# Performance work log

Hardware: AMD Instinct MI355X
Metric: run time of the kernel (lower is better)

The kernel has to match this reference:

```python
import jax, jax.numpy as jnp
import numpy as np

B, N = 2, 1024
DIM, HEADS, DH, MLP = 768, 12, 64, 3072
PD = 768          # channels * patch_size^2 = 3*16*16
GRID = 16         # image_size // patch_size
DEPTH = 8
INNER = HEADS * DH


def layer_norm(x, g):
    # torch F.layer_norm with beta=0 buffer, eps=1e-5
    m = x.mean(-1, keepdims=True)
    v = ((x - m) ** 2).mean(-1, keepdims=True)
    return (x - m) / jnp.sqrt(v + 1e-5) * g


def qk_rmsnorm(x, g):
    # F.normalize(x, dim=-1) * sqrt(DH) * gamma ; gamma is [H,1,DH]
    n = jnp.linalg.norm(x, axis=-1, keepdims=True)
    return x / jnp.maximum(n, 1e-12) * (DH ** 0.5) * g


def setup_inputs() -> dict:
    key = jax.random.key(0)
    ks = jax.random.split(key, 16)
    s = 0.02
    d = {
        "patches": jax.random.normal(ks[0], (B, N, PD), dtype=jnp.float32),
        "h_idx": jax.random.randint(ks[1], (B, N), 0, GRID),
        "w_idx": jax.random.randint(ks[2], (B, N), 0, GRID),
        "image_ids": jnp.sort(jax.random.randint(ks[3], (B, N), 0, 8), axis=-1),
        "pos_h": jax.random.normal(ks[4], (GRID, PD)) * s,
        "pos_w": jax.random.normal(ks[5], (GRID, PD)) * s,
        "Wp": jax.random.normal(ks[6], (PD, DIM)) * s,
        "bp": jnp.zeros((DIM,)),
        "ln_p": jnp.ones((DIM,)),
        "ln1": jnp.ones((DEPTH, DIM)),
        "qg": jnp.ones((DEPTH, HEADS, 1, DH)),
        "kg": jnp.ones((DEPTH, HEADS, 1, DH)),
        "Wq": jax.random.normal(ks[7], (DEPTH, DIM, INNER)) * s,
        "Wkv": jax.random.normal(ks[8], (DEPTH, DIM, 2 * INNER)) * s,
        "Wo": jax.random.normal(ks[9], (DEPTH, INNER, DIM)) * s,
        "ln2": jnp.ones((DEPTH, DIM)),
        "W1": jax.random.normal(ks[10], (DEPTH, DIM, MLP)) * s,
        "b1": jnp.zeros((DEPTH, MLP)),
        "W2": jax.random.normal(ks[11], (DEPTH, MLP, DIM)) * s,
        "b2": jnp.zeros((DEPTH, DIM)),
        "lnf": jnp.ones((DIM,)),
    }
    return d


def reference(patches, h_idx, w_idx, image_ids, pos_h, pos_w, Wp, bp, ln_p,
              ln1, qg, kg, Wq, Wkv, Wo, ln2, W1, b1, W2, b2, lnf):
    # pos embed added to raw patches before projection (pos_embed_before_proj=True)
    x = patches + pos_h[h_idx] + pos_w[w_idx]            # [B,N,PD]
    x = layer_norm(x @ Wp + bp, ln_p)                    # [B,N,DIM]

    # block-diagonal attn_mask: tokens attend only within their own packed image
    mask = image_ids[:, None, :, None] == image_ids[:, None, None, :]  # [B,1,N,N]

    for i in range(DEPTH):
        xn = layer_norm(x, ln1[i])
        q = (xn @ Wq[i]).reshape(B, N, HEADS, DH).transpose(0, 2, 1, 3)
        k, v = jnp.split(xn @ Wkv[i], 2, axis=-1)
        k = k.reshape(B, N, HEADS, DH).transpose(0, 2, 1, 3)
        v = v.reshape(B, N, HEADS, DH).transpose(0, 2, 1, 3)
        q = qk_rmsnorm(q, qg[i])
        k = qk_rmsnorm(k, kg[i])
        dots = jnp.einsum('bhid,bhjd->bhij', q, k)       # [B,H,N,N]
        dots = jnp.where(mask, dots, -jnp.finfo(dots.dtype).max)
        attn = jax.nn.softmax(dots, axis=-1)
        o = jnp.einsum('bhij,bhjd->bhid', attn, v)
        o = o.transpose(0, 2, 1, 3).reshape(B, N, INNER)
        x = o @ Wo[i] + x
        h = jax.nn.gelu(layer_norm(x, ln2[i]) @ W1[i] + b1[i], approximate=False)
        x = (h @ W2[i] + b2[i]) + x
    return layer_norm(x, lnf)
```

## Files before the change

### kernel.cpp

```cpp
#include <hip/hip_runtime.h>
#include <hip/hip_bf16.h>
#include <math.h>

typedef _Float16 f16;
typedef f16   f16x8 __attribute__((ext_vector_type(8)));
typedef float f32x4 __attribute__((ext_vector_type(4)));
typedef unsigned short ushort_t;

#define DIM   768
#define HEADS 12
#define DH    64
#define MLP_  3072
#define NTOK  2048
#define SEQ   1024
#define WELTS 7077888

__device__ __forceinline__ ushort_t h2u(f16 h){ return __builtin_bit_cast(ushort_t, h); }
__device__ __forceinline__ unsigned pk2h(float a, float b){
  return (unsigned)h2u((f16)a) | ((unsigned)h2u((f16)b) << 16);
}
__device__ __forceinline__ void gload16(const void* g, void* l){
  __builtin_amdgcn_global_load_lds(
      (const __attribute__((address_space(1))) void*)g,
      (__attribute__((address_space(3))) void*)l, 16, 0, 0);
}
__device__ __forceinline__ float wred_sum(float v){
  #pragma unroll
  for (int o = 32; o > 0; o >>= 1) v += __shfl_xor(v, o);
  return v;
}

__global__ __launch_bounds__(256) void convert_w_kernel(
    const float* __restrict__ Wq, const float* __restrict__ Wkv,
    const float* __restrict__ Wo, const float* __restrict__ W1,
    const float* __restrict__ W2, int layer, int wp_only,
    f16* __restrict__ th)
{
  int bid = blockIdx.x;
  const float* src; int K, N; size_t ooff; int t;
  if (wp_only){ src = Wq; K = 768; N = 768; ooff = 0; t = bid; }
  else if (bid < 288) { src = Wq;  K = 768;  N = 768;  ooff = 0;       t = bid; }
  else if (bid < 864) { src = Wkv; K = 768;  N = 1536; ooff = 589824;  t = bid - 288; }
  else if (bid < 1152){ src = Wo;  K = 768;  N = 768;  ooff = 1769472; t = bid - 864; }
  else if (bid < 2304){ src = W1;  K = 768;  N = 3072; ooff = 2359296; t = bid - 1152; }
  else                { src = W2;  K = 3072; N = 768;  ooff = 4718592; t = bid - 2304; }
  if (!wp_only) src += (size_t)layer * K * N;
  int ntn = N >> 6;
  int tk = t / ntn, tn = t % ntn;
  int k0 = tk * 32, n0 = tn * 64;

  __shared__ ushort_t lh[32][66];
  int tid = threadIdx.x;
  #pragma unroll
  for (int rr = 0; rr < 2; rr++){
    int k = rr * 16 + (tid >> 4);
    int n = (tid & 15) * 4;
    float4 v = *(const float4*)(src + (size_t)(k0 + k) * N + n0 + n);
    lh[k][n+0] = h2u((f16)v.x); lh[k][n+1] = h2u((f16)v.y);
    lh[k][n+2] = h2u((f16)v.z); lh[k][n+3] = h2u((f16)v.w);
  }
  __syncthreads();
  int n = tid >> 2, kq = tid & 3;
  unsigned ph[4];
  #pragma unroll
  for (int j = 0; j < 4; j++)
    ph[j] = (unsigned)lh[kq*8 + 2*j][n] | ((unsigned)lh[kq*8 + 2*j + 1][n] << 16);
  size_t obase = ooff + (size_t)(n0 + n) * K + k0 + kq * 8;
  *(uint4*)(th + obase) = make_uint4(ph[0], ph[1], ph[2], ph[3]);
}

__global__ __launch_bounds__(256) void gemm_big(
    const f16* __restrict__ Aq, const f16* __restrict__ Bw,
    const float* __restrict__ bias,
    float* __restrict__ C, f16* __restrict__ Cq,
    f16* __restrict__ Qh, f16* __restrict__ Kt, f16* __restrict__ Vt,
    const float* __restrict__ qgam, const float* __restrict__ kgam,
    int N, int K, int nbx, int mode)
{
  __shared__ __align__(16) f16 sA[128 * 64];
  __shared__ __align__(16) f16 sB[128 * 64];
  const int tid = threadIdx.x;
  const int wid = tid >> 6, lane = tid & 63;
  const int nwg = nbx << 4;
  const int bid = blockIdx.x;
  const int swz = (bid & 7) * (nwg >> 3) + (bid >> 3);
  const int by = swz & 15, bx = swz >> 4;
  const int brow = by << 7, bcol = bx << 7;
  const int m2 = wid & 1, n2 = wid >> 1;
  const int fr = lane & 15, fq = lane >> 4;
  const int Kc = K / (int)gridDim.z;
  const int kbase = (int)blockIdx.z * Kc;
  const int nk = Kc >> 6;

  const f16* pA = Aq + (size_t)brow * K + kbase;
  const f16* pB = Bw + (size_t)bcol * K + kbase;

  f32x4 acc[4][4] = {};

  for (int ks = 0; ks < nk; ks++){
    const int k0 = ks << 6;
    if (ks) __syncthreads();
    #pragma unroll
    for (int i = 0; i < 4; i++){
      int idx = tid + i * 256;
      int r = idx >> 3, c = idx & 7;
      int gc = c ^ (r & 7);
      gload16(pA + (size_t)r * K + k0 + gc * 8, &sA[idx * 8]);
      gload16(pB + (size_t)r * K + k0 + gc * 8, &sB[idx * 8]);
    }
    __syncthreads();
    #pragma unroll
    for (int s = 0; s < 2; s++){
      f16x8 a[4], b[4];
      #pragma unroll
      for (int m = 0; m < 4; m++){
        int r = m2 * 64 + m * 16 + fr;
        int ch = (s * 4 + fq) ^ (r & 7);
        a[m] = *(const f16x8*)(&sA[r * 64 + ch * 8]);
      }
      #pragma unroll
      for (int n = 0; n < 4; n++){
        int r = n2 * 64 + n * 16 + fr;
        int ch = (s * 4 + fq) ^ (r & 7);
        b[n] = *(const f16x8*)(&sB[r * 64 + ch * 8]);
      }
      #pragma unroll
      for (int m = 0; m < 4; m++)
        #pragma unroll
        for (int n = 0; n < 4; n++)
          acc[m][n] = __builtin_amdgcn_mfma_f32_16x16x32_f16(a[m], b[n], acc[m][n], 0, 0, 0);
    }
  }

  if (mode == 2){
    const int hbase = bcol + n2 * 64;
    if (hbase < 768){
      float gp[4];
      #pragma unroll
      for (int n = 0; n < 4; n++){
        int col = hbase + n * 16 + fr;
        gp[n] = qgam[col] * kgam[col];
      }
      #pragma unroll
      for (int m = 0; m < 4; m++)
        #pragma unroll
        for (int i = 0; i < 4; i++){
          float s = 0.f;
          #pragma unroll
          for (int n = 0; n < 4; n++) s += acc[m][n][i] * acc[m][n][i];
          s += __shfl_xor(s, 1); s += __shfl_xor(s, 2);
          s += __shfl_xor(s, 4); s += __shfl_xor(s, 8);
          float f = 8.f / fmaxf(sqrtf(s), 1e-12f);
          int row = brow + m2 * 64 + m * 16 + (fq << 2) + i;
          #pragma unroll
          for (int n = 0; n < 4; n++)
            Qh[(size_t)row * 768 + hbase + n * 16 + fr] = (f16)(acc[m][n][i] * f * gp[n]);
        }
    } else if (hbase < 1536){
      int hh = (hbase - 768) >> 6;
      #pragma unroll
      for (int m = 0; m < 4; m++)
        #pragma unroll
        for (int i = 0; i < 4; i++){
          float s = 0.f;
          #pragma unroll
          for (int n = 0; n < 4; n++) s += acc[m][n][i] * acc[m][n][i];
          s += __shfl_xor(s, 1); s += __shfl_xor(s, 2);
          s += __shfl_xor(s, 4); s += __shfl_xor(s, 8);
          float f = 8.f / fmaxf(sqrtf(s), 1e-12f);
          int row = brow + m2 * 64 + m * 16 + (fq << 2) + i;
          int bq = row >> 10, tok = row & 1023;
          #pragma unroll
          for (int n = 0; n < 4; n++)
            Kt[((size_t)(bq * 12 + hh) * 1024 + tok) * 64 + n * 16 + fr]
                = (f16)(acc[m][n][i] * f);
        }
    } else {
      int hh = (hbase - 1536) >> 6;
      #pragma unroll
      for (int n = 0; n < 4; n++){
        int dd = n * 16 + fr;
        #pragma unroll
        for (int m = 0; m < 4; m++){
          int row0 = brow + m2 * 64 + m * 16 + (fq << 2);
          int bq = row0 >> 10, tok0 = row0 & 1023;
          ushort4 sv;
          sv.x = h2u((f16)acc[m][n][0]); sv.y = h2u((f16)acc[m][n][1]);
          sv.z = h2u((f16)acc[m][n][2]); sv.w = h2u((f16)acc[m][n][3]);
          *(ushort4*)(Vt + ((size_t)((bq * 12 + hh) * 64 + dd)) * 1024 + tok0) = sv;
        }
      }
    }
  } else if (mode == 1){
    #pragma unroll
    for (int n = 0; n < 4; n++){
      int col = bcol + n2 * 64 + n * 16 + fr;
      float bv = bias[col];
      #pragma unroll
      for (int m = 0; m < 4; m++){
        int row0 = brow + m2 * 64 + m * 16 + (fq << 2);
        #pragma unroll
        for (int i = 0; i < 4; i++){
          float v = acc[m][n][i] + bv;
          float ge = 0.5f * v * (1.f + erff(v * 0.70710678118654752f));
          Cq[(size_t)(row0 + i) * N + col] = (f16)ge;
        }
      }
    }
  } else {
    float* P = C + (size_t)blockIdx.z * ((size_t)NTOK * N);
    #pragma unroll
    for (int n = 0; n < 4; n++){
      int col = bcol + n2 * 64 + n * 16 + fr;
      #pragma unroll
      for (int m = 0; m < 4; m++){
        int row0 = brow + m2 * 64 + m * 16 + (fq << 2);
        #pragma unroll
        for (int i = 0; i < 4; i++)
          P[(size_t)(row0 + i) * N + col] = acc[m][n][i];
      }
    }
  }
}

__global__ __launch_bounds__(256) void gemm_small(
    const f16* __restrict__ Aq, const f16* __restrict__ Bw,
    const float* __restrict__ bias, const float* __restrict__ res,
    float* __restrict__ C, int N, int K, int nbx)
{
  __shared__ __align__(16) f16 sA[2][64 * 64];
  __shared__ __align__(16) f16 sB[2][64 * 64];
  const int tid = threadIdx.x;
  const int wid = tid >> 6, lane = tid & 63;
  const int nwg = nbx << 5;
  const int bid = blockIdx.x;
  const int swz = (bid & 7) * (nwg >> 3) + (bid >> 3);
  const int by = swz & 31, bx = swz >> 5;
  const int brow = by << 6, bcol = bx << 6;
  const int m2 = wid & 1, n2 = wid >> 1;
  const int fr = lane & 15, fq = lane >> 4;
  const int nk = K >> 6;

  const f16* pA = Aq + (size_t)brow * K;
  const f16* pB = Bw + (size_t)bcol * K;

  f32x4 acc[2][2] = {};

  auto STAGE = [&](int buf, int ks){
    const int k0 = ks << 6;
    #pragma unroll
    for (int i = 0; i < 2; i++){
      int idx = tid + i * 256;
      int r = idx >> 3, c = idx & 7;
      int gc = c ^ (r & 7);
      gload16(pA + (size_t)r * K + k0 + gc * 8, &sA[buf][idx * 8]);
      gload16(pB + (size_t)r * K + k0 + gc * 8, &sB[buf][idx * 8]);
    }
  };

  STAGE(0, 0);
  __syncthreads();
  int cur = 0;
  for (int ks = 0; ks < nk; ks++){
    if (ks + 1 < nk) STAGE(cur ^ 1, ks + 1);
    #pragma unroll
    for (int s = 0; s < 2; s++){
      f16x8 a[2], b[2];
      #pragma unroll
      for (int m = 0; m < 2; m++){
        int r = m2 * 32 + m * 16 + fr;
        int ch = (s * 4 + fq) ^ (r & 7);
        a[m] = *(const f16x8*)(&sA[cur][r * 64 + ch * 8]);
      }
      #pragma unroll
      for (int n = 0; n < 2; n++){
        int r = n2 * 32 + n * 16 + fr;
        int ch = (s * 4 + fq) ^ (r & 7);
        b[n] = *(const f16x8*)(&sB[cur][r * 64 + ch * 8]);
      }
      #pragma unroll
      for (int m = 0; m < 2; m++)
        #pragma unroll
        for (int n = 0; n < 2; n++)
          acc[m][n] = __builtin_amdgcn_mfma_f32_16x16x32_f16(a[m], b[n], acc[m][n], 0, 0, 0);
    }
    __syncthreads();
    cur ^= 1;
  }

  #pragma unroll
  for (int n = 0; n < 2; n++){
    int col = bcol + n2 * 32 + n * 16 + fr;
    float bv = bias ? bias[col] : 0.f;
    #pragma unroll
    for (int m = 0; m < 2; m++){
      int row0 = brow + m2 * 32 + m * 16 + (fq << 2);
      #pragma unroll
      for (int i = 0; i < 4; i++){
        float v = acc[m][n][i] + bv;
        size_t o = (size_t)(row0 + i) * N + col;
        if (res) v += res[o];
        C[o] = v;
      }
    }
  }
}

__global__ __launch_bounds__(256) void lnred_kernel(
    float* __restrict__ x, const float* __restrict__ p, const float* __restrict__ badd,
    int npart, const float* __restrict__ g, f16* __restrict__ yq, float* __restrict__ yf)
{
  int wid = threadIdx.x >> 6, lane = threadIdx.x & 63;
  int row = blockIdx.x * 4 + wid;
  float* xr = x + (size_t)row * DIM;
  float v[12]; float s = 0.f;
  if (npart){
    #pragma unroll
    for (int d = 0; d < 12; d++){
      int c = d * 64 + lane;
      float t = xr[c] + badd[c];
      for (int j = 0; j < 4; j++)
        t += p[(size_t)j * (NTOK * DIM) + (size_t)row * DIM + c];
      xr[c] = t; v[d] = t; s += t;
    }
  } else {
    #pragma unroll
    for (int d = 0; d < 12; d++){ v[d] = xr[d * 64 + lane]; s += v[d]; }
  }
  s = wred_sum(s);
  float mean = s * (1.f / 768.f);
  float q2 = 0.f;
  #pragma unroll
  for (int d = 0; d < 12; d++){ float t = v[d] - mean; q2 += t * t; }
  q2 = wred_sum(q2);
  float rstd = rsqrtf(q2 * (1.f / 768.f) + 1e-5f);
  size_t base = (size_t)row * DIM;
  #pragma unroll
  for (int d = 0; d < 12; d++){
    float y = (v[d] - mean) * rstd * g[d * 64 + lane];
    if (yq) yq[base + d * 64 + lane] = (f16)y;
    else    yf[base + d * 64 + lane] = y;
  }
}

__global__ __launch_bounds__(256) void posadd_kernel(
    const float* __restrict__ patches, const int* __restrict__ hi,
    const int* __restrict__ wi, const float* __restrict__ ph,
    const float* __restrict__ pw, f16* __restrict__ oq)
{
  int idx = blockIdx.x * 256 + threadIdx.x;
  int tok = idx / 192, cv = idx % 192;
  float4 p = ((const float4*)patches)[idx];
  float4 a = *(const float4*)(ph + (size_t)hi[tok] * DIM + cv * 4);
  float4 b = *(const float4*)(pw + (size_t)wi[tok] * DIM + cv * 4);
  ushort4 o;
  o.x = h2u((f16)(p.x + a.x + b.x)); o.y = h2u((f16)(p.y + a.y + b.y));
  o.z = h2u((f16)(p.z + a.z + b.z)); o.w = h2u((f16)(p.w + a.w + b.w));
  ((ushort4*)oq)[idx] = o;
}

__global__ void seg_kernel(const int* __restrict__ ids, int2* __restrict__ segs)
{
  int i = blockIdx.x * 256 + threadIdx.x;
  int b = blockIdx.y;
  const int* row = ids + b * SEQ;
  int v = row[i];
  int lo = 0, hi = SEQ;
  while (lo < hi){ int mid = (lo + hi) >> 1; if (row[mid] <  v) lo = mid + 1; else hi = mid; }
  int s = lo;
  lo = 0; hi = SEQ;
  while (lo < hi){ int mid = (lo + hi) >> 1; if (row[mid] <= v) lo = mid + 1; else hi = mid; }
  segs[b * SEQ + i] = make_int2(s, lo);
}

__global__ __launch_bounds__(256) void attn_kernel(
    const f16* __restrict__ qh, const f16* __restrict__ ktp,
    const f16* __restrict__ vt, const int2* __restrict__ segs,
    f16* __restrict__ oq)
{
  __shared__ __align__(16) ushort_t Kq[32 * 64];
  __shared__ __align__(16) ushort_t Vl[64 * 40];

  const int tid = threadIdx.x;
  const int w = tid >> 6, lane = tid & 63;
  const int q15 = lane & 15, kg = lane >> 4;
  const int bh = blockIdx.x, b = bh / 12, h = bh % 12;
  const int qt = blockIdx.y;
  const int qrow = qt * 64 + w * 16 + q15;
  const size_t qtok = (size_t)b * SEQ + qrow;

  const f16* qp = qh + qtok * DIM + h * 64 + kg * 8;
  f16x8 qf[2];
  qf[0] = *(const f16x8*)(qp);
  qf[1] = *(const f16x8*)(qp + 32);

  const int2 se  = segs[qtok];
  const int2 se0 = segs[(size_t)b * SEQ + qt * 64];
  const int2 se1 = segs[(size_t)b * SEQ + qt * 64 + 63];
  const int klo = se0.x & ~31, khi = se1.y;

  float m = -3.0e38f, l = 0.f;
  f32x4 oacc[4] = {};

  const int krl = tid >> 3, kcl = tid & 7;
  const int kgc = kcl ^ (krl & 7);
  const f16* kbase = ktp + (size_t)bh * 1024 * 64;
  const int vd = tid >> 2, vko = (tid & 3) * 8;

  for (int kt0 = klo; kt0 < khi; kt0 += 32){
    gload16(kbase + (size_t)(kt0 + krl) * 64 + kgc * 8, Kq + tid * 8);
    {
      int ksrc = kt0 + vko;
      uint4 vv = *(const uint4*)(vt + ((size_t)bh * 64 + vd) * SEQ + ksrc);
      *(uint4*)((char*)Vl + vd * 80 + vko * 2) = vv;
    }
    __syncthreads();

    f32x4 s[2] = {};
    #pragma unroll
    for (int dh2 = 0; dh2 < 2; dh2++){
      #pragma unroll
      for (int khf = 0; khf < 2; khf++){
        int row = khf * 16 + q15;
        unsigned off = ((unsigned)row << 7) + ((unsigned)(dh2 * 4 + kg) << 4);
        off ^= (unsigned)(row & 7) << 4;
        f16x8 kf = *(const f16x8*)((const char*)Kq + off);
        s[khf] = __builtin_amdgcn_mfma_f32_16x16x32_f16(kf, qf[dh2], s[khf], 0, 0, 0);
      }
    }

    float p[8]; float tmax = -3.0e38f;
    #pragma unroll
    for (int khf = 0; khf < 2; khf++)
      #pragma unroll
      for (int i = 0; i < 4; i++){
        int key = kt0 + khf * 16 + kg * 4 + i;
        bool val = (key >= se.x) && (key < se.y);
        float sv = val ? s[khf][i] : -3.0e38f;
        p[khf * 4 + i] = sv;
        tmax = fmaxf(tmax, sv);
      }
    tmax = fmaxf(tmax, __shfl_xor(tmax, 16));
    tmax = fmaxf(tmax, __shfl_xor(tmax, 32));
    float mnew = fmaxf(m, tmax);
    float sc = __expf(m - mnew);
    float psum = 0.f;
    #pragma unroll
    for (int j = 0; j < 8; j++){
      float pv = (p[j] > -1.0e38f) ? __expf(p[j] - mnew) : 0.f;
      p[j] = pv; psum += pv;
    }
    psum += __shfl_xor(psum, 16);
    psum += __shfl_xor(psum, 32);
    l = l * sc + psum;
    m = mnew;
    #pragma unroll
    for (int dt = 0; dt < 4; dt++) oacc[dt] *= sc;

    unsigned u00 = pk2h(p[0], p[1]), u01 = pk2h(p[2], p[3]);
    unsigned u10 = pk2h(p[4], p[5]), u11 = pk2h(p[6], p[7]);
    int s0l = q15 + ((kg & 1) << 5);
    int s1l = s0l + 16;
    unsigned a0 = __shfl(u00, s0l), b0 = __shfl(u01, s0l);
    unsigned a1 = __shfl(u00, s1l), b1 = __shfl(u01, s1l);
    unsigned c0 = __shfl(u10, s0l), d0 = __shfl(u11, s0l);
    unsigned c1 = __shfl(u10, s1l), d1 = __shfl(u11, s1l);
    bool hih = kg >= 2;
    f16x8 pfrag = __builtin_bit_cast(f16x8,
        make_uint4(hih ? c0 : a0, hih ? d0 : b0, hih ? c1 : a1, hih ? d1 : b1));

    #pragma unroll
    for (int dt = 0; dt < 4; dt++){
      f16x8 vf = *(const f16x8*)((const char*)Vl + (dt * 16 + q15) * 80 + kg * 16);
      oacc[dt] = __builtin_amdgcn_mfma_f32_16x16x32_f16(vf, pfrag, oacc[dt], 0, 0, 0);
    }
    __syncthreads();
  }

  float rl = 1.f / l;
  size_t obase = qtok * DIM + h * 64;
  #pragma unroll
  for (int dt = 0; dt < 4; dt++){
    ushort4 hs;
    hs.x = h2u((f16)(oacc[dt][0] * rl)); hs.y = h2u((f16)(oacc[dt][1] * rl));
    hs.z = h2u((f16)(oacc[dt][2] * rl)); hs.w = h2u((f16)(oacc[dt][3] * rl));
    *(ushort4*)(oq + obase + dt * 16 + kg * 4) = hs;
  }
}

extern "C" void kernel_launch(void* const* d_in, const int* in_sizes, int n_in,
                              void* d_out, int out_size, void* d_ws, size_t ws_size,
                              hipStream_t stream)
{
  const float* patches   = (const float*)d_in[0];
  const int*   h_idx     = (const int*)d_in[1];
  const int*   w_idx     = (const int*)d_in[2];
  const int*   image_ids = (const int*)d_in[3];
  const float* pos_h = (const float*)d_in[4];
  const float* pos_w = (const float*)d_in[5];
  const float* Wp  = (const float*)d_in[6];
  const float* bp  = (const float*)d_in[7];
  const float* lnp = (const float*)d_in[8];
  const float* ln1 = (const float*)d_in[9];
  const float* qg  = (const float*)d_in[10];
  const float* kg  = (const float*)d_in[11];
  const float* Wq  = (const float*)d_in[12];
  const float* Wkv = (const float*)d_in[13];
  const float* Wo  = (const float*)d_in[14];
  const float* ln2 = (const float*)d_in[15];
  const float* W1  = (const float*)d_in[16];
  const float* b1  = (const float*)d_in[17];
  const float* W2  = (const float*)d_in[18];
  const float* b2  = (const float*)d_in[19];
  const float* lnf = (const float*)d_in[20];
  float* out = (float*)d_out;

  float* ws = (float*)d_ws;
  float* x    = ws;
  float* pbuf = x + NTOK * DIM;
  f16* qh  = (f16*)(pbuf + 4 * NTOK * DIM);
  f16* ktb = qh  + NTOK * DIM;
  f16* vtb = ktb + NTOK * DIM;
  f16* aAq = vtb + NTOK * DIM;
  f16* aBq = aAq + NTOK * DIM;
  f16* wth = aBq + NTOK * MLP_;
  int2* segs = (int2*)(wth + WELTS);

  seg_kernel<<<dim3(4, 2), 256, 0, stream>>>(image_ids, segs);
  posadd_kernel<<<1536, 256, 0, stream>>>(patches, h_idx, w_idx, pos_h, pos_w, aAq);
  convert_w_kernel<<<288, 256, 0, stream>>>(Wp, nullptr, nullptr, nullptr, nullptr, 0, 1, wth);
  gemm_small<<<384, 256, 0, stream>>>(aAq, wth, bp, nullptr, pbuf, DIM, DIM, 12);
  lnred_kernel<<<NTOK / 4, 256, 0, stream>>>(pbuf, nullptr, nullptr, 0, lnp, nullptr, x);

  for (int i = 0; i < 8; i++){
    convert_w_kernel<<<3456, 256, 0, stream>>>(Wq, Wkv, Wo, W1, W2, i, 0, wth);
    lnred_kernel<<<NTOK / 4, 256, 0, stream>>>(
        x, pbuf, i ? (b2 + (i - 1) * DIM) : nullptr, i ? 4 : 0,
        ln1 + i * DIM, aAq, nullptr);
    gemm_big<<<288, 256, 0, stream>>>(
        aAq, wth, nullptr, nullptr, nullptr, qh, ktb, vtb,
        qg + i * DIM, kg + i * DIM, 3 * DIM, DIM, 18, 2);
    attn_kernel<<<dim3(24, 16), 256, 0, stream>>>(qh, ktb, vtb, segs, aAq);
    gemm_small<<<384, 256, 0, stream>>>(
        aAq, wth + 1769472, nullptr, x, x, DIM, DIM, 12);
    lnred_kernel<<<NTOK / 4, 256, 0, stream>>>(
        x, nullptr, nullptr, 0, ln2 + i * DIM, aAq, nullptr);
    gemm_big<<<384, 256, 0, stream>>>(
        aAq, wth + 2359296, b1 + i * MLP_, nullptr, aBq, nullptr, nullptr, nullptr,
        nullptr, nullptr, MLP_, DIM, 24, 1);
    gemm_big<<<dim3(96, 1, 4), 256, 0, stream>>>(
        aBq, wth + 4718592, nullptr, pbuf, nullptr, nullptr, nullptr, nullptr,
        nullptr, nullptr, DIM, MLP_, 6, 3);
  }
  lnred_kernel<<<NTOK / 4, 256, 0, stream>>>(x, pbuf, b2 + 7 * DIM, 4, lnf, nullptr, out);
}
```

Baseline: 979.2 us.

## Preconvert all layer weights once, widen gemm_big to 512 threads, fp16 split-K partials

When the workspace is large enough, all eight layers' weights are converted to fp16 in one batched launch instead of one conversion launch per layer. gemm_big now runs 8 waves per block, each owning a 32x64 sub-tile, so more waves share each LDS tile and each holds fewer accumulators. The W2 split-K drops from 4 to 3 slices and writes fp16 partials, which the layernorm-reduce kernel reads. This cuts launch count and partial-sum traffic, at the cost of lower precision in the partial sums and a larger workspace footprint.

```diff
diff --git a/kernel.cpp b/kernel.cpp
--- a/kernel.cpp
+++ b/kernel.cpp
@@ -37,6 +37,8 @@
     f16* __restrict__ th)
 {
   int bid = blockIdx.x;
+  size_t lws = 0;
+  if (layer < 0){ layer = bid / 3456; bid -= layer * 3456; lws = (size_t)layer * WELTS; }
   const float* src; int K, N; size_t ooff; int t;
   if (wp_only){ src = Wq; K = 768; N = 768; ooff = 0; t = bid; }
   else if (bid < 288) { src = Wq;  K = 768;  N = 768;  ooff = 0;       t = bid; }
@@ -65,14 +67,14 @@
   #pragma unroll
   for (int j = 0; j < 4; j++)
     ph[j] = (unsigned)lh[kq*8 + 2*j][n] | ((unsigned)lh[kq*8 + 2*j + 1][n] << 16);
-  size_t obase = ooff + (size_t)(n0 + n) * K + k0 + kq * 8;
+  size_t obase = lws + ooff + (size_t)(n0 + n) * K + k0 + kq * 8;
   *(uint4*)(th + obase) = make_uint4(ph[0], ph[1], ph[2], ph[3]);
 }
 
-__global__ __launch_bounds__(256) void gemm_big(
+__global__ __launch_bounds__(512) void gemm_big(
     const f16* __restrict__ Aq, const f16* __restrict__ Bw,
     const float* __restrict__ bias,
-    float* __restrict__ C, f16* __restrict__ Cq,
+    f16* __restrict__ Cq,
     f16* __restrict__ Qh, f16* __restrict__ Kt, f16* __restrict__ Vt,
     const float* __restrict__ qgam, const float* __restrict__ kgam,
     int N, int K, int nbx, int mode)
@@ -86,7 +88,7 @@
   const int swz = (bid & 7) * (nwg >> 3) + (bid >> 3);
   const int by = swz & 15, bx = swz >> 4;
   const int brow = by << 7, bcol = bx << 7;
-  const int m2 = wid & 1, n2 = wid >> 1;
+  const int wr = (wid & 3) << 5, wc = (wid >> 2) << 6;
   const int fr = lane & 15, fq = lane >> 4;
   const int Kc = K / (int)gridDim.z;
   const int kbase = (int)blockIdx.z * Kc;
@@ -95,14 +97,14 @@
   const f16* pA = Aq + (size_t)brow * K + kbase;
   const f16* pB = Bw + (size_t)bcol * K + kbase;
 
-  f32x4 acc[4][4] = {};
+  f32x4 acc[2][4] = {};
 
   for (int ks = 0; ks < nk; ks++){
     const int k0 = ks << 6;
     if (ks) __syncthreads();
     #pragma unroll
-    for (int i = 0; i < 4; i++){
-      int idx = tid + i * 256;
+    for (int i = 0; i < 2; i++){
+      int idx = tid + i * 512;
       int r = idx >> 3, c = idx & 7;
       int gc = c ^ (r & 7);
       gload16(pA + (size_t)r * K + k0 + gc * 8, &sA[idx * 8]);
@@ -111,21 +113,21 @@
     __syncthreads();
     #pragma unroll
     for (int s = 0; s < 2; s++){
-      f16x8 a[4], b[4];
-      #pragma unroll
-      for (int m = 0; m < 4; m++){
-        int r = m2 * 64 + m * 16 + fr;
+      f16x8 a[2], b[4];
+      #pragma unroll
+      for (int m = 0; m < 2; m++){
+        int r = wr + m * 16 + fr;
         int ch = (s * 4 + fq) ^ (r & 7);
         a[m] = *(const f16x8*)(&sA[r * 64 + ch * 8]);
       }
       #pragma unroll
       for (int n = 0; n < 4; n++){
-        int r = n2 * 64 + n * 16 + fr;
+        int r = wc + n * 16 + fr;
         int ch = (s * 4 + fq) ^ (r & 7);
         b[n] = *(const f16x8*)(&sB[r * 64 + ch * 8]);
       }
       #pragma unroll
-      for (int m = 0; m < 4; m++)
+      for (int m = 0; m < 2; m++)
         #pragma unroll
         for (int n = 0; n < 4; n++)
           acc[m][n] = __builtin_amdgcn_mfma_f32_16x16x32_f16(a[m], b[n], acc[m][n], 0, 0, 0);
@@ -133,7 +135,7 @@
   }
 
   if (mode == 2){
-    const int hbase = bcol + n2 * 64;
+    const int hbase = bcol + wc;
     if (hbase < 768){
       float gp[4];
       #pragma unroll
@@ -142,7 +144,7 @@
         gp[n] = qgam[col] * kgam[col];
       }
       #pragma unroll
-      for (int m = 0; m < 4; m++)
+      for (int m = 0; m < 2; m++)
         #pragma unroll
         for (int i = 0; i < 4; i++){
           float s = 0.f;
@@ -151,7 +153,7 @@
           s += __shfl_xor(s, 1); s += __shfl_xor(s, 2);
           s += __shfl_xor(s, 4); s += __shfl_xor(s, 8);
           float f = 8.f / fmaxf(sqrtf(s), 1e-12f);
-          int row = brow + m2 * 64 + m * 16 + (fq << 2) + i;
+          int row = brow + wr + m * 16 + (fq << 2) + i;
           #pragma unroll
           for (int n = 0; n < 4; n++)
             Qh[(size_t)row * 768 + hbase + n * 16 + fr] = (f16)(acc[m][n][i] * f * gp[n]);
@@ -159,7 +161,7 @@
     } else if (hbase < 1536){
       int hh = (hbase - 768) >> 6;
       #pragma unroll
-      for (int m = 0; m < 4; m++)
+      for (int m = 0; m < 2; m++)
         #pragma unroll
         for (int i = 0; i < 4; i++){
           float s = 0.f;
@@ -168,7 +170,7 @@
           s += __shfl_xor(s, 1); s += __shfl_xor(s, 2);
           s += __shfl_xor(s, 4); s += __shfl_xor(s, 8);
           float f = 8.f / fmaxf(sqrtf(s), 1e-12f);
-          int row = brow + m2 * 64 + m * 16 + (fq << 2) + i;
+          int row = brow + wr + m * 16 + (fq << 2) + i;
           int bq = row >> 10, tok = row & 1023;
           #pragma unroll
           for (int n = 0; n < 4; n++)
@@ -181,8 +183,8 @@
       for (int n = 0; n < 4; n++){
         int dd = n * 16 + fr;
         #pragma unroll
-        for (int m = 0; m < 4; m++){
-          int row0 = brow + m2 * 64 + m * 16 + (fq << 2);
+        for (int m = 0; m < 2; m++){
+          int row0 = brow + wr + m * 16 + (fq << 2);
           int bq = row0 >> 10, tok0 = row0 & 1023;
           ushort4 sv;
           sv.x = h2u((f16)acc[m][n][0]); sv.y = h2u((f16)acc[m][n][1]);
@@ -194,11 +196,11 @@
   } else if (mode == 1){
     #pragma unroll
     for (int n = 0; n < 4; n++){
-      int col = bcol + n2 * 64 + n * 16 + fr;
+      int col = bcol + wc + n * 16 + fr;
       float bv = bias[col];
       #pragma unroll
-      for (int m = 0; m < 4; m++){
-        int row0 = brow + m2 * 64 + m * 16 + (fq << 2);
+      for (int m = 0; m < 2; m++){
+        int row0 = brow + wr + m * 16 + (fq << 2);
         #pragma unroll
         for (int i = 0; i < 4; i++){
           float v = acc[m][n][i] + bv;
@@ -208,16 +210,16 @@
       }
     }
   } else {
-    float* P = C + (size_t)blockIdx.z * ((size_t)NTOK * N);
+    f16* P = Cq + (size_t)blockIdx.z * ((size_t)NTOK * N);
     #pragma unroll
     for (int n = 0; n < 4; n++){
-      int col = bcol + n2 * 64 + n * 16 + fr;
-      #pragma unroll
-      for (int m = 0; m < 4; m++){
-        int row0 = brow + m2 * 64 + m * 16 + (fq << 2);
+      int col = bcol + wc + n * 16 + fr;
+      #pragma unroll
+      for (int m = 0; m < 2; m++){
+        int row0 = brow + wr + m * 16 + (fq << 2);
         #pragma unroll
         for (int i = 0; i < 4; i++)
-          P[(size_t)(row0 + i) * N + col] = acc[m][n][i];
+          P[(size_t)(row0 + i) * N + col] = (f16)acc[m][n][i];
       }
     }
   }
@@ -307,7 +309,7 @@
 }
 
 __global__ __launch_bounds__(256) void lnred_kernel(
-    float* __restrict__ x, const float* __restrict__ p, const float* __restrict__ badd,
+    float* __restrict__ x, const f16* __restrict__ p, const float* __restrict__ badd,
     int npart, const float* __restrict__ g, f16* __restrict__ yq, float* __restrict__ yf)
 {
   int wid = threadIdx.x >> 6, lane = threadIdx.x & 63;
@@ -319,8 +321,8 @@
     for (int d = 0; d < 12; d++){
       int c = d * 64 + lane;
       float t = xr[c] + badd[c];
-      for (int j = 0; j < 4; j++)
-        t += p[(size_t)j * (NTOK * DIM) + (size_t)row * DIM + c];
+      for (int j = 0; j < npart; j++)
+        t += (float)p[(size_t)j * (NTOK * DIM) + (size_t)row * DIM + c];
       xr[c] = t; v[d] = t; s += t;
     }
   } else {
@@ -515,42 +517,49 @@
   const float* lnf = (const float*)d_in[20];
   float* out = (float*)d_out;
 
-  float* ws = (float*)d_ws;
-  float* x    = ws;
-  float* pbuf = x + NTOK * DIM;
-  f16* qh  = (f16*)(pbuf + 4 * NTOK * DIM);
-  f16* ktb = qh  + NTOK * DIM;
-  f16* vtb = ktb + NTOK * DIM;
-  f16* aAq = vtb + NTOK * DIM;
-  f16* aBq = aAq + NTOK * DIM;
-  f16* wth = aBq + NTOK * MLP_;
-  int2* segs = (int2*)(wth + WELTS);
+  char* w = (char*)d_ws;
+  float* x = (float*)w;            w += (size_t)NTOK * DIM * 4;
+  f16* pbufh = (f16*)w;            w += (size_t)3 * NTOK * DIM * 2;
+  f16* qh  = (f16*)w;              w += (size_t)NTOK * DIM * 2;
+  f16* ktb = (f16*)w;              w += (size_t)NTOK * DIM * 2;
+  f16* vtb = (f16*)w;              w += (size_t)NTOK * DIM * 2;
+  f16* aAq = (f16*)w;              w += (size_t)NTOK * DIM * 2;
+  f16* aBq = (f16*)w;              w += (size_t)NTOK * MLP_ * 2;
+  int2* segs = (int2*)w;           w += (size_t)NTOK * 8;
+  f16* wall = (f16*)w;
+  size_t base_used = (size_t)(w - (char*)d_ws);
+  const bool pre = ws_size >= base_used + (size_t)8 * WELTS * 2;
+  float* ptmp = (float*)aBq;
 
   seg_kernel<<<dim3(4, 2), 256, 0, stream>>>(image_ids, segs);
   posadd_kernel<<<1536, 256, 0, stream>>>(patches, h_idx, w_idx, pos_h, pos_w, aAq);
-  convert_w_kernel<<<288, 256, 0, stream>>>(Wp, nullptr, nullptr, nullptr, nullptr, 0, 1, wth);
-  gemm_small<<<384, 256, 0, stream>>>(aAq, wth, bp, nullptr, pbuf, DIM, DIM, 12);
-  lnred_kernel<<<NTOK / 4, 256, 0, stream>>>(pbuf, nullptr, nullptr, 0, lnp, nullptr, x);
+  convert_w_kernel<<<288, 256, 0, stream>>>(Wp, nullptr, nullptr, nullptr, nullptr, 0, 1, wall);
+  gemm_small<<<384, 256, 0, stream>>>(aAq, wall, bp, nullptr, ptmp, DIM, DIM, 12);
+  lnred_kernel<<<NTOK / 4, 256, 0, stream>>>(ptmp, nullptr, nullptr, 0, lnp, nullptr, x);
+  if (pre)
+    convert_w_kernel<<<27648, 256, 0, stream>>>(Wq, Wkv, Wo, W1, W2, -1, 0, wall);
 
   for (int i = 0; i < 8; i++){
-    convert_w_kernel<<<3456, 256, 0, stream>>>(Wq, Wkv, Wo, W1, W2, i, 0, wth);
+    f16* wl = wall + (pre ? (size_t)i * WELTS : 0);
+    if (!pre)
+      convert_w_kernel<<<3456, 256, 0, stream>>>(Wq, Wkv, Wo, W1, W2, i, 0, wall);
     lnred_kernel<<<NTOK / 4, 256, 0, stream>>>(
-        x, pbuf, i ? (b2 + (i - 1) * DIM) : nullptr, i ? 4 : 0,
+        x, pbufh, i ? (b2 + (i - 1) * DIM) : nullptr, i ? 3 : 0,
         ln1 + i * DIM, aAq, nullptr);
-    gemm_big<<<288, 256, 0, stream>>>(
-        aAq, wth, nullptr, nullptr, nullptr, qh, ktb, vtb,
+    gemm_big<<<288, 512, 0, stream>>>(
+        aAq, wl, nullptr, nullptr, qh, ktb, vtb,
         qg + i * DIM, kg + i * DIM, 3 * DIM, DIM, 18, 2);
     attn_kernel<<<dim3(24, 16), 256, 0, stream>>>(qh, ktb, vtb, segs, aAq);
     gemm_small<<<384, 256, 0, stream>>>(
-        aAq, wth + 1769472, nullptr, x, x, DIM, DIM, 12);
+        aAq, wl + 1769472, nullptr, x, x, DIM, DIM, 12);
     lnred_kernel<<<NTOK / 4, 256, 0, stream>>>(
         x, nullptr, nullptr, 0, ln2 + i * DIM, aAq, nullptr);
-    gemm_big<<<384, 256, 0, stream>>>(
-        aAq, wth + 2359296, b1 + i * MLP_, nullptr, aBq, nullptr, nullptr, nullptr,
+    gemm_big<<<384, 512, 0, stream>>>(
+        aAq, wl + 2359296, b1 + i * MLP_, aBq, nullptr, nullptr, nullptr,
         nullptr, nullptr, MLP_, DIM, 24, 1);
-    gemm_big<<<dim3(96, 1, 4), 256, 0, stream>>>(
-        aBq, wth + 4718592, nullptr, pbuf, nullptr, nullptr, nullptr, nullptr,
+    gemm_big<<<dim3(96, 1, 3), 512, 0, stream>>>(
+        aBq, wl + 4718592, nullptr, pbufh, nullptr, nullptr, nullptr,
         nullptr, nullptr, DIM, MLP_, 6, 3);
   }
-  lnred_kernel<<<NTOK / 4, 256, 0, stream>>>(x, pbuf, b2 + 7 * DIM, 4, lnf, nullptr, out);
-}
+  lnred_kernel<<<NTOK / 4, 256, 0, stream>>>(x, pbufh, b2 + 7 * DIM, 3, lnf, nullptr, out);
+}
```

Measured after the change: 1.074 ms. +9.7%, slower.
